# Optimization experiments

Measured on AMD Instinct MI355X. Metric: run time of the kernel, lower is better.

## Reference

```python
import jax, jax.numpy as jnp
import numpy as np

B, KL, XL, DIM, H, PB = 4, 128, 4096, 256, 8, 8
HD = DIM // H
SCALE = HD ** -0.5
N_DIS = 64 + 2


def setup_inputs() -> dict:
    key = jax.random.key(0)
    ks = jax.random.split(key, 10)
    x = jax.random.normal(ks[0], (B, XL, DIM), jnp.float32)
    kernal = jax.random.normal(ks[1], (B, KL, DIM), jnp.float32)
    rd = jax.random.randint(ks[2], (B, KL, XL), 0, N_DIS)
    polar_pos = jax.random.randint(ks[3], (B, KL, XL), 0, PB)
    att_mask = jax.random.uniform(ks[4], (B, H, XL, KL)) < 0.1
    W_qkv = jax.random.normal(ks[5], (DIM, 3 * DIM), jnp.float32) * 0.02
    dis_embed = jax.random.normal(ks[6], (N_DIS, H), jnp.float32) * 0.02
    polar_emb = jax.random.normal(ks[7], (PB, 1), jnp.float32) * 0.02
    W_proj = jax.random.normal(ks[8], (DIM, DIM), jnp.float32) * 0.02
    b_proj = jnp.zeros((DIM,), jnp.float32)
    return dict(x=x, kernal=kernal, rd=rd, polar_pos=polar_pos, att_mask=att_mask,
                W_qkv=W_qkv, dis_embed=dis_embed, polar_emb=polar_emb,
                W_proj=W_proj, b_proj=b_proj)


def _heads(t, h):
    b, n, d = t.shape
    return t.reshape(b, n, h, d // h).transpose(0, 2, 1, 3)  # b h n hd


def reference(x, kernal, rd, polar_pos, att_mask, W_qkv, dis_embed, polar_emb, W_proj, b_proj):
    b, xl, dim = x.shape
    kl = kernal.shape[1]
    h = H
    scale = (dim // h) ** -0.5

    q, k, v = [_heads(t, h) for t in jnp.split(x @ W_qkv, 3, axis=-1)]        # b h xl hd
    k_q, k_k, k_v = [_heads(t, h) for t in jnp.split(kernal @ W_qkv, 3, axis=-1)]  # b h kl hd

    rd_e = dis_embed[rd].transpose(0, 3, 1, 2)  # (b,kl,xl,h) -> (b,h,kl,xl)

    # kernel -> x attention scores
    k_x_attn = jnp.einsum('bhkd,bhxd->bhkx', k_q, k) * scale  # b h kl xl

    # main orientation: one-hot-weighted |attn| reduced over x, argmax over polar bins
    pp = jnp.broadcast_to(polar_pos[:, None], (b, h, kl, xl))  # b h kl xl
    polar_hot = jax.nn.one_hot(pp, PB, dtype=k_x_attn.dtype)   # b h kl xl o
    ori_sum = jnp.einsum('bhkx,bhkxo->bhko', jnp.abs(k_x_attn), polar_hot)
    main_ori = jnp.argmax(ori_sum, axis=-1)                    # b h kl
    new_polar = pp - main_ori[..., None]
    new_polar = jnp.where(new_polar < 0, new_polar + PB, new_polar)
    polar_bias = polar_emb[new_polar, 0]                       # b h kl xl

    mask_k = att_mask.transpose(0, 1, 3, 2)                    # b h kl xl
    k_x_attn = jnp.where(mask_k, jnp.asarray(-1e6, k_x_attn.dtype), k_x_attn)
    attn_k = jax.nn.softmax(k_x_attn + rd_e + polar_bias, axis=-1)
    k_out = jnp.einsum('bhkx,bhxd->bhkd', attn_k, v)
    k_out = k_out.transpose(0, 2, 1, 3).reshape(b, kl, dim) @ W_proj + b_proj

    # x -> kernel attention scores
    x_k_attn = jnp.einsum('bhxd,bhkd->bhxk', q, k_k) * scale   # b h xl kl
    x_k_attn = jnp.where(att_mask, jnp.asarray(-1e9, x_k_attn.dtype), x_k_attn)
    x_k_attn = jax.nn.softmax(x_k_attn + rd_e.transpose(0, 1, 3, 2)
                              + polar_bias.transpose(0, 1, 3, 2), axis=-1)
    x_out = jnp.einsum('bhxk,bhkd->bhxd', x_k_attn, k_v)
    x_out = x_out.transpose(0, 2, 1, 3).reshape(b, xl, dim) @ W_proj + b_proj

    return (x_out, k_out)
```

## Files before the change

### kernel.cpp

```cpp
#include <hip/hip_runtime.h>
#include <hip/hip_bf16.h>

#define B_    4
#define KL_   128
#define XL_   4096
#define DIM_  256
#define H_    8
#define HD_   32
#define PB_   8
#define NDIS_ 66
#define TDIM_ 768
#define SCALE_ 0.17677669529663687f
#define XT_   64
#define KC_   8
#define NS_   4
#define XCH_  (XL_ / NS_)
#define NCH_  64

typedef float v4f __attribute__((ext_vector_type(4)));
typedef short v8s __attribute__((ext_vector_type(8)));

__device__ __forceinline__ unsigned short f2bf(float f) {
    __hip_bfloat16 h = __float2bfloat16(f);
    return __builtin_bit_cast(unsigned short, h);
}
__device__ __forceinline__ float bf2f(unsigned short u) {
    return __bfloat162float(__builtin_bit_cast(__hip_bfloat16, u));
}
__device__ __forceinline__ void cvt_hilo(float v, unsigned short& hi, unsigned short& lo) {
    hi = f2bf(v);
    lo = f2bf(v - bf2f(hi));
}

__global__ __launch_bounds__(256) void cvt_mat(const float* __restrict__ A,
                                               unsigned short* __restrict__ Ah,
                                               unsigned short* __restrict__ Al,
                                               size_t n4) {
    size_t i = ((size_t)blockIdx.x * 256 + threadIdx.x);
    if (i >= n4) return;
    float4 v = *(const float4*)&A[i * 4];
    ushort4 h, l;
    cvt_hilo(v.x, h.x, l.x);
    cvt_hilo(v.y, h.y, l.y);
    cvt_hilo(v.z, h.z, l.z);
    cvt_hilo(v.w, h.w, l.w);
    *(ushort4*)&Ah[i * 4] = h;
    *(ushort4*)&Al[i * 4] = l;
}

__global__ __launch_bounds__(256) void cvt_wT(const float* __restrict__ W,
                                              unsigned short* __restrict__ Wh,
                                              unsigned short* __restrict__ Wl,
                                              int K, int N) {
    int n = blockIdx.x, k = threadIdx.x;
    float v = W[(size_t)k * N + n];
    unsigned short h, l;
    cvt_hilo(v, h, l);
    Wh[(size_t)n * K + k] = h;
    Wl[(size_t)n * K + k] = l;
}

__global__ __launch_bounds__(256) void cvt_kq(const float* __restrict__ qkv_k,
                                              unsigned short* __restrict__ Kqh_g,
                                              unsigned short* __restrict__ Kql_g) {
    const int bh = blockIdx.x;
    const int b = bh >> 3, h = bh & 7;
    const int tid = threadIdx.x;
    const int k = tid >> 1, dg = (tid & 1) * 16;
    const float* src = &qkv_k[((size_t)(b * KL_ + k)) * TDIM_ + h * HD_ + dg];
    unsigned short hi[16], lo[16];
#pragma unroll
    for (int j4 = 0; j4 < 4; ++j4) {
        float4 v = *(const float4*)&src[j4 * 4];
        cvt_hilo(v.x, hi[j4 * 4 + 0], lo[j4 * 4 + 0]);
        cvt_hilo(v.y, hi[j4 * 4 + 1], lo[j4 * 4 + 1]);
        cvt_hilo(v.z, hi[j4 * 4 + 2], lo[j4 * 4 + 2]);
        cvt_hilo(v.w, hi[j4 * 4 + 3], lo[j4 * 4 + 3]);
    }
    unsigned short* dh = &Kqh_g[((size_t)bh * KL_ + k) * HD_ + dg];
    unsigned short* dl = &Kql_g[((size_t)bh * KL_ + k) * HD_ + dg];
    *(uint4*)&dh[0] = *(uint4*)&hi[0];
    *(uint4*)&dh[8] = *(uint4*)&hi[8];
    *(uint4*)&dl[0] = *(uint4*)&lo[0];
    *(uint4*)&dl[8] = *(uint4*)&lo[8];
}

__global__ __launch_bounds__(256) void gemm_mfma(const unsigned short* __restrict__ Ah,
                                                 const unsigned short* __restrict__ Al,
                                                 const unsigned short* __restrict__ Bh,
                                                 const unsigned short* __restrict__ Bl,
                                                 float* __restrict__ C,
                                                 const float* __restrict__ bias,
                                                 int M, int N, int K) {
    __shared__ __align__(16) unsigned short Ah_s[128][40];
    __shared__ __align__(16) unsigned short Al_s[128][40];
    __shared__ __align__(16) unsigned short Bh_s[128][40];
    __shared__ __align__(16) unsigned short Bl_s[128][40];
    const int tid = threadIdx.x;
    const int w = tid >> 6, lane = tid & 63;
    const int c = lane & 15, q = lane >> 4;
    const int bm = blockIdx.y * 128, bn = blockIdx.x * 128;
    const int srow = tid >> 1, shf = (tid & 1) * 16;

    v4f acc[2][8] = {};
    for (int k0 = 0; k0 < K; k0 += 32) {
        __syncthreads();
        {
            const size_t ab = (size_t)(bm + srow) * K + k0 + shf;
            *(uint4*)&Ah_s[srow][shf] = *(const uint4*)&Ah[ab];
            *(uint4*)&Ah_s[srow][shf + 8] = *(const uint4*)&Ah[ab + 8];
            *(uint4*)&Al_s[srow][shf] = *(const uint4*)&Al[ab];
            *(uint4*)&Al_s[srow][shf + 8] = *(const uint4*)&Al[ab + 8];
            const size_t bb = (size_t)(bn + srow) * K + k0 + shf;
            *(uint4*)&Bh_s[srow][shf] = *(const uint4*)&Bh[bb];
            *(uint4*)&Bh_s[srow][shf + 8] = *(const uint4*)&Bh[bb + 8];
            *(uint4*)&Bl_s[srow][shf] = *(const uint4*)&Bl[bb];
            *(uint4*)&Bl_s[srow][shf + 8] = *(const uint4*)&Bl[bb + 8];
        }
        __syncthreads();
        v8s afh[2], afl[2];
#pragma unroll
        for (int mt = 0; mt < 2; ++mt) {
            afh[mt] = *(v8s*)&Ah_s[w * 32 + mt * 16 + c][q * 8];
            afl[mt] = *(v8s*)&Al_s[w * 32 + mt * 16 + c][q * 8];
        }
#pragma unroll
        for (int nt = 0; nt < 8; ++nt) {
            v8s bfh = *(v8s*)&Bh_s[nt * 16 + c][q * 8];
            v8s bfl = *(v8s*)&Bl_s[nt * 16 + c][q * 8];
#pragma unroll
            for (int mt = 0; mt < 2; ++mt) {
                acc[mt][nt] = __builtin_amdgcn_mfma_f32_16x16x32_bf16(afl[mt], bfh, acc[mt][nt], 0, 0, 0);
                acc[mt][nt] = __builtin_amdgcn_mfma_f32_16x16x32_bf16(afh[mt], bfl, acc[mt][nt], 0, 0, 0);
                acc[mt][nt] = __builtin_amdgcn_mfma_f32_16x16x32_bf16(afh[mt], bfh, acc[mt][nt], 0, 0, 0);
            }
        }
    }
#pragma unroll
    for (int mt = 0; mt < 2; ++mt) {
#pragma unroll
        for (int nt = 0; nt < 8; ++nt) {
            int col = bn + nt * 16 + c;
            float bv = bias ? bias[col] : 0.0f;
#pragma unroll
            for (int r = 0; r < 4; ++r) {
                int row = bm + w * 32 + mt * 16 + q * 4 + r;
                C[(size_t)row * N + col] = acc[mt][nt][r] + bv;
            }
        }
    }
}

__global__ __launch_bounds__(256) void gemm64(const float* __restrict__ A,
                                              const float* __restrict__ Bw,
                                              float* __restrict__ C,
                                              const float* __restrict__ bias,
                                              int M, int N, int K) {
    __shared__ __align__(16) float As[16][68];
    __shared__ __align__(16) float Bs[16][64];
    const int tid = threadIdx.x;
    const int tx = tid & 15, ty = tid >> 4;
    const int bn = blockIdx.x * 64, bm = blockIdx.y * 64;
    const int am = tid >> 2, ac = tid & 3;
    float acc[4][4] = {};
    for (int k0 = 0; k0 < K; k0 += 16) {
        float4 a4 = *(const float4*)&A[(size_t)(bm + am) * K + k0 + ac * 4];
        As[ac * 4 + 0][am] = a4.x;
        As[ac * 4 + 1][am] = a4.y;
        As[ac * 4 + 2][am] = a4.z;
        As[ac * 4 + 3][am] = a4.w;
        *(float4*)&Bs[ty][tx * 4] = *(const float4*)&Bw[(size_t)(k0 + ty) * N + bn + tx * 4];
        __syncthreads();
#pragma unroll
        for (int kk = 0; kk < 16; ++kk) {
            float4 av = *(const float4*)&As[kk][ty * 4];
            float4 bv = *(const float4*)&Bs[kk][tx * 4];
            float a[4] = {av.x, av.y, av.z, av.w};
            float b[4] = {bv.x, bv.y, bv.z, bv.w};
#pragma unroll
            for (int i = 0; i < 4; ++i)
#pragma unroll
                for (int j = 0; j < 4; ++j) acc[i][j] += a[i] * b[j];
        }
        __syncthreads();
    }
#pragma unroll
    for (int i = 0; i < 4; ++i) {
        int m = bm + ty * 4 + i;
#pragma unroll
        for (int j = 0; j < 4; ++j) {
            int n = bn + tx * 4 + j;
            float v = acc[i][j];
            if (bias) v += bias[n];
            C[(size_t)m * N + n] = v;
        }
    }
}

__global__ __launch_bounds__(256) void score_bins_mfma2(const float* __restrict__ qkv_x,
                                                        const unsigned short* __restrict__ Kqh_g,
                                                        const unsigned short* __restrict__ Kql_g,
                                                        const int* __restrict__ rd,
                                                        const int* __restrict__ polar_pos,
                                                        const int* __restrict__ att_mask,
                                                        const float* __restrict__ dis_embed,
                                                        __hip_bfloat16* __restrict__ Sg,
                                                        float* __restrict__ binspart) {
    const int b = blockIdx.z, h = blockIdx.y, xc = blockIdx.x;
    const int x0 = xc * 64;
    const int tid = threadIdx.x;
    const int w = tid >> 6, lane = tid & 63;
    const int c15 = lane & 15, q = lane >> 4;
    const size_t bh = (size_t)(b * H_ + h);

    __shared__ __align__(16) unsigned short Kqh_s[KL_][40];
    __shared__ __align__(16) unsigned short Kql_s[KL_][40];
    __shared__ unsigned int mskb[64][5];
    __shared__ float de_h[NDIS_];
    __shared__ float binsL[8][4][16][PB_];

    {
        int k = tid >> 1, dg = (tid & 1) * 16;
        const unsigned short* sh = &Kqh_g[(bh * KL_ + k) * HD_ + dg];
        const unsigned short* sl = &Kql_g[(bh * KL_ + k) * HD_ + dg];
        *(uint4*)&Kqh_s[k][dg] = *(const uint4*)&sh[0];
        *(uint4*)&Kqh_s[k][dg + 8] = *(const uint4*)&sh[8];
        *(uint4*)&Kql_s[k][dg] = *(const uint4*)&sl[0];
        *(uint4*)&Kql_s[k][dg + 8] = *(const uint4*)&sl[8];
    }
    {
        int xr = tid >> 2, kg = tid & 3;
        size_t gb = (bh * XL_ + x0 + xr) * KL_ + kg * 32;
        unsigned bits = 0;
#pragma unroll
        for (int i = 0; i < 8; ++i) {
            int4 m4 = *(const int4*)&att_mask[gb + i * 4];
            bits |= (m4.x ? 1u : 0u) << (i * 4 + 0);
            bits |= (m4.y ? 1u : 0u) << (i * 4 + 1);
            bits |= (m4.z ? 1u : 0u) << (i * 4 + 2);
            bits |= (m4.w ? 1u : 0u) << (i * 4 + 3);
        }
        mskb[xr][kg] = bits;
    }
    if (tid < NDIS_) de_h[tid] = dis_embed[tid * H_ + h];
    __syncthreads();

    v8s axh, axl;
    {
        const float* src = &qkv_x[((size_t)b * XL_ + x0 + w * 16 + c15) * TDIM_ + DIM_ + h * HD_ + q * 8];
        float4 v0 = *(const float4*)&src[0];
        float4 v1 = *(const float4*)&src[4];
        float vv[8] = {v0.x, v0.y, v0.z, v0.w, v1.x, v1.y, v1.z, v1.w};
#pragma unroll
        for (int j = 0; j < 8; ++j) {
            unsigned short hi, lo;
            cvt_hilo(vv[j], hi, lo);
            ((short*)&axh)[j] = (short)hi;
            ((short*)&axl)[j] = (short)lo;
        }
    }

    const int xw = x0 + w * 16;

#pragma unroll
    for (int nt = 0; nt < 8; ++nt) {
        const int k = nt * 16 + c15;
        v8s bqh = *(v8s*)&Kqh_s[k][q * 8];
        v8s bql = *(v8s*)&Kql_s[k][q * 8];
        v4f D = {0.f, 0.f, 0.f, 0.f};
        D = __builtin_amdgcn_mfma_f32_16x16x32_bf16(axl, bqh, D, 0, 0, 0);
        D = __builtin_amdgcn_mfma_f32_16x16x32_bf16(axh, bql, D, 0, 0, 0);
        D = __builtin_amdgcn_mfma_f32_16x16x32_bf16(axh, bqh, D, 0, 0, 0);

        const size_t rowoff = ((size_t)(b * KL_ + k)) * XL_ + xw + q * 4;
        int4 r4 = *(const int4*)&rd[rowoff];
        int4 p4 = *(const int4*)&polar_pos[rowoff];
        int rv[4] = {r4.x, r4.y, r4.z, r4.w};
        int pv[4] = {p4.x, p4.y, p4.z, p4.w};

        float bins[PB_] = {};
        ushort4 pack;
#pragma unroll
        for (int r = 0; r < 4; ++r) {
            float s = D[r] * SCALE_;
            float a = fabsf(s);
            int pp = pv[r];
#pragma unroll
            for (int pb = 0; pb < PB_; ++pb) bins[pb] += (pp == pb) ? a : 0.0f;
            int xloc = w * 16 + q * 4 + r;
            int mbit = (mskb[xloc][k >> 5] >> (k & 31)) & 1;
            float sp = (mbit ? -1e6f : s) + de_h[rv[r]];
            ((unsigned short*)&pack)[r] = f2bf(sp);
        }
        *(ushort4*)((unsigned short*)Sg + (bh * KL_ + k) * XL_ + xw + q * 4) = pack;

#pragma unroll
        for (int pb = 0; pb < PB_; ++pb) {
            bins[pb] += __shfl_xor(bins[pb], 16);
            bins[pb] += __shfl_xor(bins[pb], 32);
        }
        if (q == 0) {
#pragma unroll
            for (int pb = 0; pb < PB_; ++pb) binsL[nt][w][c15][pb] = bins[pb];
        }
    }
    __syncthreads();
    {
        int k = tid >> 1, half = tid & 1;
        int nt = k >> 4, c = k & 15;
        float4 s = {0.f, 0.f, 0.f, 0.f};
#pragma unroll
        for (int w4 = 0; w4 < 4; ++w4) {
            float4 v = *(float4*)&binsL[nt][w4][c][half * 4];
            s.x += v.x; s.y += v.y; s.z += v.z; s.w += v.w;
        }
        *(float4*)&binspart[(bh * KL_ + k) * (NCH_ * PB_) + xc * PB_ + half * 4] = s;
    }
}

__global__ __launch_bounds__(256) void bins_argmax(const float* __restrict__ binspart,
                                                   int* __restrict__ main_ori) {
    const int w = threadIdx.x >> 6, lane = threadIdx.x & 63;
    const int row = blockIdx.x * 4 + w;
    const float* bp = &binspart[(size_t)row * (NCH_ * PB_) + lane * PB_];
    float s[PB_];
#pragma unroll
    for (int pb = 0; pb < PB_; ++pb) s[pb] = bp[pb];
#pragma unroll
    for (int m = 1; m < 64; m <<= 1)
#pragma unroll
        for (int pb = 0; pb < PB_; ++pb) s[pb] += __shfl_xor(s[pb], m);
    if (lane == 0) {
        float best = s[0];
        int bi = 0;
#pragma unroll
        for (int pb = 1; pb < PB_; ++pb)
            if (s[pb] > best) { best = s[pb]; bi = pb; }
        main_ori[row] = bi;
    }
}

__global__ __launch_bounds__(256) void flash_cached(const float* __restrict__ qkv_x,
                                                    const __hip_bfloat16* __restrict__ Sg,
                                                    const int* __restrict__ polar_pos,
                                                    const float* __restrict__ polar_emb,
                                                    const int* __restrict__ main_ori,
                                                    float* __restrict__ part) {
    const int b = blockIdx.z, h = blockIdx.y;
    const int kch = blockIdx.x / NS_, xc = blockIdx.x % NS_;
    const int k0 = kch * KC_;
    const int tid = threadIdx.x;
    const int ki = tid >> 5, xt = tid & 31;

    __shared__ __align__(16) float4 vs[XT_][9];
    __shared__ int pol_s[KC_][68];
    __shared__ float pe[PB_];

    if (tid < PB_) pe[tid] = polar_emb[tid];
    const size_t xbase = (size_t)b * XL_;
    const size_t bh = (size_t)(b * H_ + h);
    const size_t row_k = bh * KL_ + k0 + ki;
    const int mo = main_ori[row_k];
    const int xbeg = xc * XCH_;

    float l = 0.f;
    float4 acc[8] = {};
    __syncthreads();
    for (int t = 0; t < XCH_ / XT_; ++t) {
        const int x0 = xbeg + t * XT_;
        __syncthreads();
#pragma unroll
        for (int i = 0; i < 2; ++i) {
            int id = tid + 256 * i;
            int row = id >> 3, c = id & 7;
            vs[row][c] = *(const float4*)&qkv_x[(xbase + x0 + row) * TDIM_ + 2 * DIM_ + h * HD_ + c * 4];
        }
        if (tid < 128) {
            int kk = tid >> 4, c = tid & 15;
            *(int4*)&pol_s[kk][c * 4] =
                *(const int4*)&polar_pos[(size_t)(b * KL_ + k0 + kk) * XL_ + x0 + c * 4];
        }
        __syncthreads();
#pragma unroll
        for (int j = 0; j < 2; ++j) {
            int xl = xt + 32 * j;
            int x = x0 + xl;
            float sp = __bfloat162float(Sg[row_k * XL_ + x]);
            int pp = pol_s[ki][xl];
            int np = pp - mo;
            np += (np >> 31) & PB_;
            float p = __expf(sp + pe[np]);
            l += p;
#pragma unroll
            for (int c = 0; c < 8; ++c) {
                float4 v = vs[xl][c];
                acc[c].x += p * v.x; acc[c].y += p * v.y;
                acc[c].z += p * v.z; acc[c].w += p * v.w;
            }
        }
    }
#pragma unroll
    for (int m = 1; m < 32; m <<= 1) {
        l += __shfl_xor(l, m);
#pragma unroll
        for (int c = 0; c < 8; ++c) {
            acc[c].x += __shfl_xor(acc[c].x, m);
            acc[c].y += __shfl_xor(acc[c].y, m);
            acc[c].z += __shfl_xor(acc[c].z, m);
            acc[c].w += __shfl_xor(acc[c].w, m);
        }
    }
    if (xt == 0) {
        float* dst = &part[(size_t)(row_k * NS_ + xc) * 36];
#pragma unroll
        for (int c = 0; c < 8; ++c) *(float4*)&dst[c * 4] = acc[c];
        dst[32] = l;
    }
}

__global__ __launch_bounds__(256) void merge_cached(const float* __restrict__ part,
                                                    float* __restrict__ kout_pre) {
    const int tid = threadIdx.x;
    const int ri = tid >> 5, d = tid & 31;
    const int row = blockIdx.x * 8 + ri;
    float l = 0.f, a = 0.f;
#pragma unroll
    for (int c = 0; c < NS_; ++c) {
        const float* p = &part[(size_t)(row * NS_ + c) * 36];
        l += p[32];
        a += p[d];
    }
    int k = row & (KL_ - 1);
    int bh = row >> 7;
    int h = bh & (H_ - 1), b = bh >> 3;
    kout_pre[(size_t)(b * KL_ + k) * DIM_ + h * HD_ + d] = a / l;
}

__global__ __launch_bounds__(256) void attn_x_mfma(const float* __restrict__ qkv_x,
                                                   const float* __restrict__ qkv_k,
                                                   const int* __restrict__ rd,
                                                   const int* __restrict__ polar_pos,
                                                   const int* __restrict__ att_mask,
                                                   const float* __restrict__ dis_embed,
                                                   const float* __restrict__ polar_emb,
                                                   const int* __restrict__ main_ori,
                                                   float* __restrict__ xout_pre) {
    const int b = blockIdx.z, h = blockIdx.y;
    const int x0 = blockIdx.x * 64;
    const int tid = threadIdx.x;
    const int wave = tid >> 6, lane = tid & 63;
    const int c = lane & 15, q = lane >> 4;

    __shared__ __align__(16) unsigned short Kk_s[KL_][40];
    __shared__ __align__(16) unsigned short VT_s[HD_][136];
    __shared__ __align__(16) unsigned short P_s[4][16][136];
    __shared__ unsigned short rp_s[KL_][72];
    __shared__ float de_h[NDIS_];
    __shared__ float pe[PB_];
    __shared__ int mo_s[KL_];

    const size_t bh = (size_t)(b * H_ + h);
    if (tid < NDIS_) de_h[tid] = dis_embed[tid * H_ + h];
    if (tid < PB_) pe[tid] = polar_emb[tid];
    if (tid < KL_) mo_s[tid] = main_ori[bh * KL_ + tid];

    {
        int row = tid >> 1, half = tid & 1;
        const float* src = &qkv_k[(size_t)(b * KL_ + row) * TDIM_ + h * HD_ + half * 16];
#pragma unroll
        for (int j = 0; j < 16; ++j) Kk_s[row][half * 16 + j] = f2bf(src[DIM_ + j]);
#pragma unroll
        for (int j = 0; j < 16; ++j) VT_s[half * 16 + j][row] = f2bf(src[2 * DIM_ + j]);
    }
    __syncthreads();

#pragma unroll
    for (int i = 0; i < 8; ++i) {
        int id = tid + 256 * i;
        int k = id >> 4, cc = id & 15;
        size_t gb = (size_t)(b * KL_ + k) * XL_ + x0 + cc * 4;
        int4 r4 = *(const int4*)&rd[gb];
        int4 p4 = *(const int4*)&polar_pos[gb];
        int mo = mo_s[k];
        int n0 = p4.x - mo; n0 += (n0 >> 31) & PB_;
        int n1 = p4.y - mo; n1 += (n1 >> 31) & PB_;
        int n2 = p4.z - mo; n2 += (n2 >> 31) & PB_;
        int n3 = p4.w - mo; n3 += (n3 >> 31) & PB_;
        rp_s[k][cc * 4 + 0] = (unsigned short)(r4.x | (n0 << 8));
        rp_s[k][cc * 4 + 1] = (unsigned short)(r4.y | (n1 << 8));
        rp_s[k][cc * 4 + 2] = (unsigned short)(r4.z | (n2 << 8));
        rp_s[k][cc * 4 + 3] = (unsigned short)(r4.w | (n3 << 8));
    }
    __syncthreads();
#pragma unroll
    for (int i = 0; i < 8; ++i) {
        int id = tid + 256 * i;
        int xr = id >> 5, kc = id & 31;
        int4 m4 = *(const int4*)&att_mask[(bh * XL_ + x0 + xr) * KL_ + kc * 4];
        if (m4.x) rp_s[kc * 4 + 0][xr] |= 0x8000;
        if (m4.y) rp_s[kc * 4 + 1][xr] |= 0x8000;
        if (m4.z) rp_s[kc * 4 + 2][xr] |= 0x8000;
        if (m4.w) rp_s[kc * 4 + 3][xr] |= 0x8000;
    }
    __syncthreads();

    v8s aq;
    {
        const float* qp = &qkv_x[(size_t)(b * XL_ + x0 + wave * 16 + c) * TDIM_ + h * HD_ + q * 8];
        float4 q0 = *(const float4*)&qp[0];
        float4 q1 = *(const float4*)&qp[4];
        aq[0] = (short)f2bf(q0.x); aq[1] = (short)f2bf(q0.y);
        aq[2] = (short)f2bf(q0.z); aq[3] = (short)f2bf(q0.w);
        aq[4] = (short)f2bf(q1.x); aq[5] = (short)f2bf(q1.y);
        aq[6] = (short)f2bf(q1.z); aq[7] = (short)f2bf(q1.w);
    }

    v4f S[8];
#pragma unroll
    for (int t = 0; t < 8; ++t) {
        v8s bk = *(v8s*)&Kk_s[t * 16 + c][q * 8];
        S[t] = __builtin_amdgcn_mfma_f32_16x16x32_bf16(aq, bk, (v4f){0.f, 0.f, 0.f, 0.f}, 0, 0, 0);
    }

    const int xloc = wave * 16;
    float lr[4] = {0.f, 0.f, 0.f, 0.f};
#pragma unroll
    for (int t = 0; t < 8; ++t) {
#pragma unroll
        for (int r = 0; r < 4; ++r) {
            int krow = t * 16 + c;
            int xrow = q * 4 + r;
            unsigned short rp = rp_s[krow][xloc + xrow];
            float sval = S[t][r] * SCALE_;
            float tval = ((rp & 0x8000) ? -25.0f : sval) + de_h[rp & 0x7f] + pe[(rp >> 8) & 7];
            float p = __expf(tval);
            unsigned short pb = f2bf(p);
            P_s[wave][xrow][krow] = pb;
            lr[r] += bf2f(pb);
        }
    }
#pragma unroll
    for (int r = 0; r < 4; ++r) {
#pragma unroll
        for (int m = 1; m < 16; m <<= 1) lr[r] += __shfl_xor(lr[r], m);
    }
    __syncthreads();

    v4f O0 = {0.f, 0.f, 0.f, 0.f}, O1 = {0.f, 0.f, 0.f, 0.f};
#pragma unroll
    for (int kc = 0; kc < 4; ++kc) {
        v8s ap = *(v8s*)&P_s[wave][c][kc * 32 + q * 8];
        v8s bv0 = *(v8s*)&VT_s[c][kc * 32 + q * 8];
        v8s bv1 = *(v8s*)&VT_s[16 + c][kc * 32 + q * 8];
        O0 = __builtin_amdgcn_mfma_f32_16x16x32_bf16(ap, bv0, O0, 0, 0, 0);
        O1 = __builtin_amdgcn_mfma_f32_16x16x32_bf16(ap, bv1, O1, 0, 0, 0);
    }

#pragma unroll
    for (int r = 0; r < 4; ++r) {
        int xg = x0 + wave * 16 + q * 4 + r;
        float inv = 1.0f / lr[r];
        float* op = &xout_pre[(size_t)(b * XL_ + xg) * DIM_ + h * HD_];
        op[c] = O0[r] * inv;
        op[16 + c] = O1[r] * inv;
    }
}

extern "C" void kernel_launch(void* const* d_in, const int* in_sizes, int n_in,
                              void* d_out, int out_size, void* d_ws, size_t ws_size,
                              hipStream_t stream) {
    const float* x         = (const float*)d_in[0];
    const float* kernal    = (const float*)d_in[1];
    const int* rd          = (const int*)d_in[2];
    const int* polar_pos   = (const int*)d_in[3];
    const int* att_mask    = (const int*)d_in[4];
    const float* W_qkv     = (const float*)d_in[5];
    const float* dis_embed = (const float*)d_in[6];
    const float* polar_emb = (const float*)d_in[7];
    const float* W_proj    = (const float*)d_in[8];
    const float* b_proj    = (const float*)d_in[9];
    float* out             = (float*)d_out;

    char* base = (char*)d_ws;
    size_t off = 0;
    auto alloc = [&](size_t bytes) { void* p = base + off; off = (off + bytes + 255) & ~255ULL; return p; };
    float* qkv_x    = (float*)alloc((size_t)B_ * XL_ * TDIM_ * 4);
    float* qkv_k    = (float*)alloc((size_t)B_ * KL_ * TDIM_ * 4);
    float* xout_pre = (float*)alloc((size_t)B_ * XL_ * DIM_ * 4);
    float* kout_pre = (float*)alloc((size_t)B_ * KL_ * DIM_ * 4);
    int* main_ori   = (int*)alloc(B_ * H_ * KL_ * 4);
    float* part     = (float*)alloc((size_t)B_ * H_ * KL_ * NS_ * 36 * 4);
    __hip_bfloat16* Sg = (__hip_bfloat16*)alloc((size_t)B_ * H_ * KL_ * XL_ * 2);
    unsigned short* wph = (unsigned short*)alloc((size_t)DIM_ * DIM_ * 2);
    unsigned short* wpl = (unsigned short*)alloc((size_t)DIM_ * DIM_ * 2);

    float* binspart = xout_pre;
    const size_t MX = (size_t)B_ * XL_;
    unsigned short* xh = (unsigned short*)Sg;
    unsigned short* xl_ = xh + MX * DIM_;
    unsigned short* wqh = (unsigned short*)part;
    unsigned short* wql = wqh + (size_t)TDIM_ * DIM_;
    unsigned short* kqh_g = wqh + 2 * (size_t)TDIM_ * DIM_;
    unsigned short* kql_g = kqh_g + (size_t)B_ * H_ * KL_ * HD_;
    unsigned short* oh = (unsigned short*)Sg;
    unsigned short* ol = oh + MX * DIM_;

    cvt_mat<<<dim3((MX * DIM_ / 4 + 255) / 256), 256, 0, stream>>>(x, xh, xl_, MX * DIM_ / 4);
    cvt_wT<<<dim3(TDIM_), DIM_, 0, stream>>>(W_qkv, wqh, wql, DIM_, TDIM_);
    cvt_wT<<<dim3(DIM_), DIM_, 0, stream>>>(W_proj, wph, wpl, DIM_, DIM_);

    gemm_mfma<<<dim3(TDIM_ / 128, MX / 128), 256, 0, stream>>>(
        xh, xl_, wqh, wql, qkv_x, nullptr, MX, TDIM_, DIM_);
    gemm64<<<dim3(TDIM_ / 64, (B_ * KL_) / 64), 256, 0, stream>>>(
        kernal, W_qkv, qkv_k, nullptr, B_ * KL_, TDIM_, DIM_);
    cvt_kq<<<dim3(B_ * H_), 256, 0, stream>>>(qkv_k, kqh_g, kql_g);

    score_bins_mfma2<<<dim3(NCH_, H_, B_), 256, 0, stream>>>(
        qkv_x, kqh_g, kql_g, rd, polar_pos, att_mask, dis_embed, Sg, binspart);
    bins_argmax<<<dim3(B_ * H_ * KL_ / 4), 256, 0, stream>>>(binspart, main_ori);
    flash_cached<<<dim3((KL_ / KC_) * NS_, H_, B_), 256, 0, stream>>>(
        qkv_x, Sg, polar_pos, polar_emb, main_ori, part);
    merge_cached<<<dim3(B_ * H_ * KL_ / 8), 256, 0, stream>>>(part, kout_pre);

    attn_x_mfma<<<dim3(XL_ / 64, H_, B_), 256, 0, stream>>>(
        qkv_x, qkv_k, rd, polar_pos, att_mask, dis_embed, polar_emb, main_ori, xout_pre);

    cvt_mat<<<dim3((MX * DIM_ / 4 + 255) / 256), 256, 0, stream>>>(xout_pre, oh, ol, MX * DIM_ / 4);
    gemm_mfma<<<dim3(DIM_ / 128, MX / 128), 256, 0, stream>>>(
        oh, ol, wph, wpl, out, b_proj, MX, DIM_, DIM_);
    gemm64<<<dim3(DIM_ / 64, (B_ * KL_) / 64), 256, 0, stream>>>(
        kout_pre, W_proj, out + (size_t)B_ * XL_ * DIM_, b_proj, B_ * KL_, DIM_, DIM_);
}
```

Before: 382.0 us.

## Fuse hi/lo split into x-attention epilogue and retile k-side flash kernel

The x->kernel attention kernel now writes its output directly as bf16 hi/lo pairs, which removes the separate cvt_mat pass and the fp32 round trip through xout_pre. The score kernel reads K-query fragments straight from global memory (L1/L2) instead of staging them in shared memory, which saves LDS and one barrier. The flash kernel handles 16 kernel rows per block with 16 threads per row instead of 8 rows with 32 threads, halving the block count and reusing each V tile across more rows. In exchange the flash kernel does more serial work per thread, and the score kernel issues repeated global loads for K.

```diff
diff --git a/kernel.cpp b/kernel.cpp
--- a/kernel.cpp
+++ b/kernel.cpp
@@ -11,11 +11,10 @@
 #define NDIS_ 66
 #define TDIM_ 768
 #define SCALE_ 0.17677669529663687f
-#define XT_   64
-#define KC_   8
 #define NS_   4
 #define XCH_  (XL_ / NS_)
 #define NCH_  64
+#define KC2_  16
 
 typedef float v4f __attribute__((ext_vector_type(4)));
 typedef short v8s __attribute__((ext_vector_type(8)));
@@ -197,7 +196,7 @@
     }
 }
 
-__global__ __launch_bounds__(256) void score_bins_mfma2(const float* __restrict__ qkv_x,
+__global__ __launch_bounds__(256) void score_bins_mfma3(const float* __restrict__ qkv_x,
                                                         const unsigned short* __restrict__ Kqh_g,
                                                         const unsigned short* __restrict__ Kql_g,
                                                         const int* __restrict__ rd,
@@ -213,21 +212,10 @@
     const int c15 = lane & 15, q = lane >> 4;
     const size_t bh = (size_t)(b * H_ + h);
 
-    __shared__ __align__(16) unsigned short Kqh_s[KL_][40];
-    __shared__ __align__(16) unsigned short Kql_s[KL_][40];
     __shared__ unsigned int mskb[64][5];
     __shared__ float de_h[NDIS_];
     __shared__ float binsL[8][4][16][PB_];
 
-    {
-        int k = tid >> 1, dg = (tid & 1) * 16;
-        const unsigned short* sh = &Kqh_g[(bh * KL_ + k) * HD_ + dg];
-        const unsigned short* sl = &Kql_g[(bh * KL_ + k) * HD_ + dg];
-        *(uint4*)&Kqh_s[k][dg] = *(const uint4*)&sh[0];
-        *(uint4*)&Kqh_s[k][dg + 8] = *(const uint4*)&sh[8];
-        *(uint4*)&Kql_s[k][dg] = *(const uint4*)&sl[0];
-        *(uint4*)&Kql_s[k][dg + 8] = *(const uint4*)&sl[8];
-    }
     {
         int xr = tid >> 2, kg = tid & 3;
         size_t gb = (bh * XL_ + x0 + xr) * KL_ + kg * 32;
@@ -265,8 +253,9 @@
 #pragma unroll
     for (int nt = 0; nt < 8; ++nt) {
         const int k = nt * 16 + c15;
-        v8s bqh = *(v8s*)&Kqh_s[k][q * 8];
-        v8s bql = *(v8s*)&Kql_s[k][q * 8];
+        const size_t kqoff = (bh * KL_ + k) * HD_ + q * 8;
+        v8s bqh = *(const v8s*)&Kqh_g[kqoff];
+        v8s bql = *(const v8s*)&Kql_g[kqoff];
         v4f D = {0.f, 0.f, 0.f, 0.f};
         D = __builtin_amdgcn_mfma_f32_16x16x32_bf16(axl, bqh, D, 0, 0, 0);
         D = __builtin_amdgcn_mfma_f32_16x16x32_bf16(axh, bql, D, 0, 0, 0);
@@ -340,20 +329,20 @@
     }
 }
 
-__global__ __launch_bounds__(256) void flash_cached(const float* __restrict__ qkv_x,
-                                                    const __hip_bfloat16* __restrict__ Sg,
-                                                    const int* __restrict__ polar_pos,
-                                                    const float* __restrict__ polar_emb,
-                                                    const int* __restrict__ main_ori,
-                                                    float* __restrict__ part) {
+__global__ __launch_bounds__(256) void flash_cached2(const float* __restrict__ qkv_x,
+                                                     const __hip_bfloat16* __restrict__ Sg,
+                                                     const int* __restrict__ polar_pos,
+                                                     const float* __restrict__ polar_emb,
+                                                     const int* __restrict__ main_ori,
+                                                     float* __restrict__ part) {
     const int b = blockIdx.z, h = blockIdx.y;
     const int kch = blockIdx.x / NS_, xc = blockIdx.x % NS_;
-    const int k0 = kch * KC_;
+    const int k0 = kch * KC2_;
     const int tid = threadIdx.x;
-    const int ki = tid >> 5, xt = tid & 31;
-
-    __shared__ __align__(16) float4 vs[XT_][9];
-    __shared__ int pol_s[KC_][68];
+    const int ki = tid >> 4, xt = tid & 15;
+
+    __shared__ __align__(16) float4 vs[64][9];
+    __shared__ int pol_s[KC2_][68];
     __shared__ float pe[PB_];
 
     if (tid < PB_) pe[tid] = polar_emb[tid];
@@ -366,8 +355,8 @@
     float l = 0.f;
     float4 acc[8] = {};
     __syncthreads();
-    for (int t = 0; t < XCH_ / XT_; ++t) {
-        const int x0 = xbeg + t * XT_;
+    for (int t = 0; t < XCH_ / 64; ++t) {
+        const int x0 = xbeg + t * 64;
         __syncthreads();
 #pragma unroll
         for (int i = 0; i < 2; ++i) {
@@ -375,15 +364,15 @@
             int row = id >> 3, c = id & 7;
             vs[row][c] = *(const float4*)&qkv_x[(xbase + x0 + row) * TDIM_ + 2 * DIM_ + h * HD_ + c * 4];
         }
-        if (tid < 128) {
+        {
             int kk = tid >> 4, c = tid & 15;
             *(int4*)&pol_s[kk][c * 4] =
                 *(const int4*)&polar_pos[(size_t)(b * KL_ + k0 + kk) * XL_ + x0 + c * 4];
         }
         __syncthreads();
 #pragma unroll
-        for (int j = 0; j < 2; ++j) {
-            int xl = xt + 32 * j;
+        for (int j = 0; j < 4; ++j) {
+            int xl = xt + 16 * j;
             int x = x0 + xl;
             float sp = __bfloat162float(Sg[row_k * XL_ + x]);
             int pp = pol_s[ki][xl];
@@ -400,14 +389,14 @@
         }
     }
 #pragma unroll
-    for (int m = 1; m < 32; m <<= 1) {
-        l += __shfl_xor(l, m);
+    for (int m = 1; m < 16; m <<= 1) {
+        l += __shfl_xor(l, m, 16);
 #pragma unroll
         for (int c = 0; c < 8; ++c) {
-            acc[c].x += __shfl_xor(acc[c].x, m);
-            acc[c].y += __shfl_xor(acc[c].y, m);
-            acc[c].z += __shfl_xor(acc[c].z, m);
-            acc[c].w += __shfl_xor(acc[c].w, m);
+            acc[c].x += __shfl_xor(acc[c].x, m, 16);
+            acc[c].y += __shfl_xor(acc[c].y, m, 16);
+            acc[c].z += __shfl_xor(acc[c].z, m, 16);
+            acc[c].w += __shfl_xor(acc[c].w, m, 16);
         }
     }
     if (xt == 0) {
@@ -444,7 +433,8 @@
                                                    const float* __restrict__ dis_embed,
                                                    const float* __restrict__ polar_emb,
                                                    const int* __restrict__ main_ori,
-                                                   float* __restrict__ xout_pre) {
+                                                   unsigned short* __restrict__ oh,
+                                                   unsigned short* __restrict__ ol) {
     const int b = blockIdx.z, h = blockIdx.y;
     const int x0 = blockIdx.x * 64;
     const int tid = threadIdx.x;
@@ -560,9 +550,16 @@
     for (int r = 0; r < 4; ++r) {
         int xg = x0 + wave * 16 + q * 4 + r;
         float inv = 1.0f / lr[r];
-        float* op = &xout_pre[(size_t)(b * XL_ + xg) * DIM_ + h * HD_];
-        op[c] = O0[r] * inv;
-        op[16 + c] = O1[r] * inv;
+        size_t obase = (size_t)(b * XL_ + xg) * DIM_ + h * HD_;
+        float v0 = O0[r] * inv;
+        float v1 = O1[r] * inv;
+        unsigned short h0, l0, h1, l1;
+        cvt_hilo(v0, h0, l0);
+        cvt_hilo(v1, h1, l1);
+        oh[obase + c] = h0;
+        ol[obase + c] = l0;
+        oh[obase + 16 + c] = h1;
+        ol[obase + 16 + c] = l1;
     }
 }
 
@@ -615,17 +612,16 @@
         kernal, W_qkv, qkv_k, nullptr, B_ * KL_, TDIM_, DIM_);
     cvt_kq<<<dim3(B_ * H_), 256, 0, stream>>>(qkv_k, kqh_g, kql_g);
 
-    score_bins_mfma2<<<dim3(NCH_, H_, B_), 256, 0, stream>>>(
+    score_bins_mfma3<<<dim3(NCH_, H_, B_), 256, 0, stream>>>(
         qkv_x, kqh_g, kql_g, rd, polar_pos, att_mask, dis_embed, Sg, binspart);
     bins_argmax<<<dim3(B_ * H_ * KL_ / 4), 256, 0, stream>>>(binspart, main_ori);
-    flash_cached<<<dim3((KL_ / KC_) * NS_, H_, B_), 256, 0, stream>>>(
+    flash_cached2<<<dim3((KL_ / KC2_) * NS_, H_, B_), 256, 0, stream>>>(
         qkv_x, Sg, polar_pos, polar_emb, main_ori, part);
     merge_cached<<<dim3(B_ * H_ * KL_ / 8), 256, 0, stream>>>(part, kout_pre);
 
     attn_x_mfma<<<dim3(XL_ / 64, H_, B_), 256, 0, stream>>>(
-        qkv_x, qkv_k, rd, polar_pos, att_mask, dis_embed, polar_emb, main_ori, xout_pre);
-
-    cvt_mat<<<dim3((MX * DIM_ / 4 + 255) / 256), 256, 0, stream>>>(xout_pre, oh, ol, MX * DIM_ / 4);
+        qkv_x, qkv_k, rd, polar_pos, att_mask, dis_embed, polar_emb, main_ori, oh, ol);
+
     gemm_mfma<<<dim3(DIM_ / 128, MX / 128), 256, 0, stream>>>(
         oh, ol, wph, wpl, out, b_proj, MX, DIM_, DIM_);
     gemm64<<<dim3(DIM_ / 64, (B_ * KL_) / 64), 256, 0, stream>>>(
```

Measured after the change: 362.7 us. 5.1% less time.
